# Kernel tuning notes

Measured on AMD Instinct MI355X. Metric: run time of the kernel, lower is better.

## Reference

```python
import jax, jax.numpy as jnp
import numpy as np

B, NW = 1024, 300
N = NW // 3          # 100 tokens (keypoints)
E = 5                # token dim after cat of PE(2): 3 + 2
H, D, L = 4, 64, 3   # heads, d_attention, layers


def setup_inputs() -> dict:
    key = jax.random.key(0)
    ks = jax.random.split(key, 8)
    s = jnp.float32(0.1)
    x = jax.random.normal(ks[0], (B, NW), dtype=jnp.float32)
    Wq = jax.random.normal(ks[1], (L, H, D, E), dtype=jnp.float32) * s  # per-head W_Q (no bias)
    Wk = jax.random.normal(ks[2], (L, H, D, E), dtype=jnp.float32) * s
    Wv = jax.random.normal(ks[3], (L, H, D, E), dtype=jnp.float32) * s
    Wo = jax.random.normal(ks[4], (L, E, H * D), dtype=jnp.float32) * s  # MHA output proj (no bias)
    Wf = jax.random.normal(ks[5], (L, E, E), dtype=jnp.float32) * s      # FFN linear
    bf = jax.random.normal(ks[6], (L, E), dtype=jnp.float32) * s
    g1 = jnp.ones((L, E), dtype=jnp.float32)
    b1 = jnp.zeros((L, E), dtype=jnp.float32)
    g2 = jnp.ones((L, E), dtype=jnp.float32)
    b2 = jnp.zeros((L, E), dtype=jnp.float32)
    return dict(x=x, Wq=Wq, Wk=Wk, Wv=Wv, Wo=Wo, Wf=Wf, bf=bf,
                g1=g1, b1=b1, g2=g2, b2=b2)


def _layer_norm(x, g, b, eps=1e-5):
    mu = jnp.mean(x, axis=-1, keepdims=True)
    var = jnp.mean((x - mu) ** 2, axis=-1, keepdims=True)  # biased, like torch LN
    return (x - mu) / jnp.sqrt(var + eps) * g + b


def reference(x, Wq, Wk, Wv, Wo, Wf, bf, g1, b1, g2, b2):
    kp = x.reshape(B, N, 3)                      # 'b (n d) -> b n d', d=3
    mask = kp[:, :, -1] > 0                      # [B,N] keypoint confidence mask
    # PositionalEncoding(d_model=2, kind='cat'): div_term=[1] -> pe=[sin(pos),cos(pos)]
    pos = jnp.arange(N, dtype=jnp.float32)
    pe = jnp.stack([jnp.sin(pos), jnp.cos(pos)], axis=-1)         # [N,2]
    out = jnp.concatenate([kp, jnp.broadcast_to(pe, (B, N, 2))], axis=-1)  # [B,N,5]
    out = jnp.where(mask[:, :, None], out, jnp.float32(0.0))      # out[~mask]=0

    pair = mask[:, None, None, :] & mask[:, None, :, None]        # [B,1,N,N]
    neg = -jnp.finfo(jnp.float32).max
    scale = jnp.float32(1.0 / np.sqrt(D))
    for l in range(L):
        # per-head projections (heads vectorized over h)
        q = jnp.einsum('bne,hde->bhnd', out, Wq[l])
        k = jnp.einsum('bne,hde->bhnd', out, Wk[l])
        v = jnp.einsum('bne,hde->bhnd', out, Wv[l])
        dots = jnp.einsum('bhid,bhjd->bhij', q, k) * scale        # [B,H,N,N]
        dots = jnp.where(pair, dots, neg)
        attn = jax.nn.softmax(dots, axis=-1)
        o = jnp.einsum('bhij,bhjd->bhid', attn, v)                # [B,H,N,D]
        o = o.transpose(0, 2, 1, 3).reshape(B, N, H * D)          # concat heads
        attn_out = o @ Wo[l].T                                    # [B,N,E]
        ln1 = _layer_norm(attn_out + out, g1[l], b1[l])
        ffn = jax.nn.relu(ln1 @ Wf[l].T + bf[l])
        out = _layer_norm(ffn + ln1, g2[l], b2[l])
    return out
```

## Files before the change

### kernel.cpp

```cpp
#include <hip/hip_runtime.h>
#include <math.h>

#define NTOK 100
#define EDIM 5
#define NH   4
#define NL   3
#define DD   64
#define BLK  256
#define LOG2E 1.4426950408889634f

__global__ void precompute_mp(const float* __restrict__ Wq,
                              const float* __restrict__ Wk,
                              const float* __restrict__ Wv,
                              const float* __restrict__ Wo,
                              float* __restrict__ mp) {
  const int blk = blockIdx.x;
  const int which = blk / 12;
  const int rem = blk % 12;
  const int l = rem / 4, h = rem % 4;
  const int t = threadIdx.x;

  __shared__ float A[320];
  __shared__ float Bsh[320];

  const float* wa = (which ? Wv : Wq) + (l*NH + h)*DD*EDIM;
  for (int r = t; r < 320; r += 64) A[r] = wa[r];
  if (which == 0) {
    const float* wk = Wk + (l*NH + h)*DD*EDIM;
    for (int r = t; r < 320; r += 64) Bsh[r] = wk[r];
  } else {
    for (int r = t; r < 320; r += 64) {
      int f = r >> 6, d = r & 63;
      Bsh[r] = Wo[(l*EDIM + f)*(NH*DD) + h*DD + d];
    }
  }
  __syncthreads();
  if (t < 25) {
    int e = t / 5, f = t % 5;
    float acc = 0.f;
    if (which == 0) {
      #pragma unroll 8
      for (int d = 0; d < DD; ++d) acc += A[d*5+e] * Bsh[d*5+f];
      acc *= 0.125f;
    } else {
      #pragma unroll 8
      for (int d = 0; d < DD; ++d) acc += A[d*5+e] * Bsh[f*64+d];
    }
    mp[which*960 + ((l*NH + h)*EDIM + e)*8 + f] = acc;
  }
}

__global__ __launch_bounds__(BLK, 1) void encoder_kernel(
    const float* __restrict__ x,
    const float* __restrict__ mp,
    const float* __restrict__ Wf,
    const float* __restrict__ bfv,
    const float* __restrict__ g1,
    const float* __restrict__ b1,
    const float* __restrict__ g2,
    const float* __restrict__ b2,
    float* __restrict__ out)
{
  const int wv   = threadIdx.x >> 6;
  const int lane = threadIdx.x & 63;
  const int b    = blockIdx.x * 4 + wv;

  __shared__ float s_mp[1920];
  __shared__ float s_st[4][NTOK+1][8];
  __shared__ int   s_cidx[4][NTOK];

  for (int r = threadIdx.x; r < 480; r += BLK)
    ((float4*)s_mp)[r] = ((const float4*)mp)[r];
  __syncthreads();

  float* st  = &s_st[wv][0][0];
  int* cidx  = s_cidx[wv];

  const float* xb = x + b*300;
  const int t1 = lane, t2 = lane + 64;
  float k0a = xb[3*t1], k1a = xb[3*t1+1], k2a = xb[3*t1+2];
  bool m1 = (k2a > 0.f);
  float k0b = 0.f, k1b = 0.f, k2b = 0.f; bool m2 = false;
  if (t2 < NTOK) {
    k0b = xb[3*t2]; k1b = xb[3*t2+1]; k2b = xb[3*t2+2];
    m2 = (k2b > 0.f);
  }
  unsigned long long bm1 = __ballot(m1);
  unsigned long long bm2 = __ballot(m2);
  const int pc1 = __popcll(bm1);
  const int nm  = pc1 + __popcll(bm2);
  const int ns  = nm + 1;
  unsigned long long below = (lane == 0) ? 0ull : ((1ull << lane) - 1ull);
  int p1 = __popcll(bm1 & below);
  int p2 = pc1 + __popcll(bm2 & below);
  if (m1) {
    *(float4*)(st + p1*8) = make_float4(k0a, k1a, k2a, sinf((float)t1));
    st[p1*8+4] = cosf((float)t1);
  }
  cidx[t1] = m1 ? p1 : nm;
  if (t2 < NTOK) {
    if (m2) {
      *(float4*)(st + p2*8) = make_float4(k0b, k1b, k2b, sinf((float)t2));
      st[p2*8+4] = cosf((float)t2);
    }
    cidx[t2] = m2 ? p2 : nm;
  }
  if (lane == 0) {
    *(float4*)(st + nm*8) = make_float4(0.f,0.f,0.f,0.f);
    st[nm*8+4] = 0.f;
  }

  const bool slow = (ns > 64);
  const int  rB   = lane + 64;
  const bool act1 = (lane < ns);
  const bool act2 = slow && (rB < ns);
  const bool rep1 = (lane == nm);
  const bool rep2 = (rB == nm);

  float o[5], o2[5] = {0,0,0,0,0};
  {
    float4 v = *(const float4*)(st + lane*8);
    o[0]=v.x; o[1]=v.y; o[2]=v.z; o[3]=v.w; o[4]=st[lane*8+4];
  }
  if (act2) {
    float4 v = *(const float4*)(st + rB*8);
    o2[0]=v.x; o2[1]=v.y; o2[2]=v.z; o2[3]=v.w; o2[4]=st[rB*8+4];
  }

  for (int l = 0; l < NL; ++l) {
    float a[NH][5], a2[NH][5], w[NH][5], w2[NH][5], ls[NH], ls2[NH];
    const float* Ml = s_mp + l*NH*40;

    #pragma unroll
    for (int h = 0; h < NH; ++h) {
      const float* Mh = Ml + h*40;
      float A0=0.f,A1=0.f,A2=0.f,A3=0.f,A4=0.f;
      #pragma unroll
      for (int e = 0; e < 5; ++e) {
        float4 mr = *(const float4*)(Mh + e*8);
        float  m4 = Mh[e*8+4];
        A0 += o[e]*mr.x; A1 += o[e]*mr.y; A2 += o[e]*mr.z; A3 += o[e]*mr.w; A4 += o[e]*m4;
      }
      a[h][0]=A0*LOG2E; a[h][1]=A1*LOG2E; a[h][2]=A2*LOG2E;
      a[h][3]=A3*LOG2E; a[h][4]=A4*LOG2E;
      ls[h] = 0.f;
      #pragma unroll
      for (int f = 0; f < 5; ++f) w[h][f] = 0.f;
    }
    if (slow) {
      #pragma unroll
      for (int h = 0; h < NH; ++h) {
        const float* Mh = Ml + h*40;
        float A0=0.f,A1=0.f,A2=0.f,A3=0.f,A4=0.f;
        #pragma unroll
        for (int e = 0; e < 5; ++e) {
          float4 mr = *(const float4*)(Mh + e*8);
          float  m4 = Mh[e*8+4];
          A0 += o2[e]*mr.x; A1 += o2[e]*mr.y; A2 += o2[e]*mr.z; A3 += o2[e]*mr.w; A4 += o2[e]*m4;
        }
        a2[h][0]=A0*LOG2E; a2[h][1]=A1*LOG2E; a2[h][2]=A2*LOG2E;
        a2[h][3]=A3*LOG2E; a2[h][4]=A4*LOG2E;
        ls2[h] = 0.f;
        #pragma unroll
        for (int f = 0; f < 5; ++f) w2[h][f] = 0.f;
      }
    }

    if (!slow) {
      #pragma unroll 2
      for (int j = 0; j < nm; ++j) {
        float4 oj4 = *(const float4*)(st + j*8);
        float  oj5 = st[j*8+4];
        float oj[5] = {oj4.x, oj4.y, oj4.z, oj4.w, oj5};
        #pragma unroll
        for (int h = 0; h < NH; ++h) {
          float s = a[h][0]*oj[0]+a[h][1]*oj[1]+a[h][2]*oj[2]+a[h][3]*oj[3]+a[h][4]*oj[4];
          float p = __builtin_amdgcn_exp2f(s);
          p = rep1 ? 1.f : p;
          ls[h] += p;
          #pragma unroll
          for (int e = 0; e < 5; ++e) w[h][e] += p*oj[e];
        }
      }
    } else {
      #pragma unroll 2
      for (int j = 0; j < nm; ++j) {
        float4 oj4 = *(const float4*)(st + j*8);
        float  oj5 = st[j*8+4];
        float oj[5] = {oj4.x, oj4.y, oj4.z, oj4.w, oj5};
        #pragma unroll
        for (int h = 0; h < NH; ++h) {
          float sA = a[h][0]*oj[0]+a[h][1]*oj[1]+a[h][2]*oj[2]+a[h][3]*oj[3]+a[h][4]*oj[4];
          float sB = a2[h][0]*oj[0]+a2[h][1]*oj[1]+a2[h][2]*oj[2]+a2[h][3]*oj[3]+a2[h][4]*oj[4];
          float pA = __builtin_amdgcn_exp2f(sA);
          float pB = __builtin_amdgcn_exp2f(sB);
          pB = rep2 ? 1.f : pB;
          ls[h] += pA; ls2[h] += pB;
          #pragma unroll
          for (int e = 0; e < 5; ++e) { w[h][e] += pA*oj[e]; w2[h][e] += pB*oj[e]; }
        }
      }
    }

    auto token_pass = [&](float* o_, float (*w_)[5], float* ls_,
                          bool isrep, bool active, int row) {
      float wext = isrep ? (float)(NTOK - nm) : 0.f;
      float c[5] = {0.f,0.f,0.f,0.f,0.f};
      const float* Pl = s_mp + 960 + l*NH*40;
      #pragma unroll
      for (int h = 0; h < NH; ++h) {
        float inv = isrep ? 0.01f : 1.f/ls_[h];
        const float* Ph = Pl + h*40;
        #pragma unroll
        for (int f = 0; f < 5; ++f) {
          float wn = (w_[h][f] + wext*o_[f]) * inv;
          float4 pr = *(const float4*)(Ph + f*8);
          float  p4 = Ph[f*8+4];
          c[0]+=wn*pr.x; c[1]+=wn*pr.y; c[2]+=wn*pr.z; c[3]+=wn*pr.w; c[4]+=wn*p4;
        }
      }
      float y[5];
      #pragma unroll
      for (int e = 0; e < 5; ++e) y[e] = o_[e] + c[e];
      float mu = 0.2f*(y[0]+y[1]+y[2]+y[3]+y[4]);
      float var = 0.f;
      #pragma unroll
      for (int e = 0; e < 5; ++e) { float d = y[e]-mu; var += d*d; }
      var *= 0.2f;
      float inv1 = 1.f/sqrtf(var + 1e-5f);
      float ln1[5];
      #pragma unroll
      for (int e = 0; e < 5; ++e) ln1[e] = (y[e]-mu)*inv1*g1[l*5+e] + b1[l*5+e];
      float rr[5];
      #pragma unroll
      for (int e = 0; e < 5; ++e) {
        float acc = bfv[l*5+e];
        #pragma unroll
        for (int f = 0; f < 5; ++f) acc += ln1[f]*Wf[(l*5+e)*5+f];
        acc = acc > 0.f ? acc : 0.f;
        rr[e] = acc + ln1[e];
      }
      float mu2 = 0.2f*(rr[0]+rr[1]+rr[2]+rr[3]+rr[4]);
      float var2 = 0.f;
      #pragma unroll
      for (int e = 0; e < 5; ++e) { float d = rr[e]-mu2; var2 += d*d; }
      var2 *= 0.2f;
      float inv2 = 1.f/sqrtf(var2 + 1e-5f);
      float n0 = (rr[0]-mu2)*inv2*g2[l*5+0] + b2[l*5+0];
      float n1 = (rr[1]-mu2)*inv2*g2[l*5+1] + b2[l*5+1];
      float n2 = (rr[2]-mu2)*inv2*g2[l*5+2] + b2[l*5+2];
      float n3 = (rr[3]-mu2)*inv2*g2[l*5+3] + b2[l*5+3];
      float n4 = (rr[4]-mu2)*inv2*g2[l*5+4] + b2[l*5+4];
      o_[0]=n0; o_[1]=n1; o_[2]=n2; o_[3]=n3; o_[4]=n4;
      if (active) {
        *(float4*)(st + row*8) = make_float4(n0,n1,n2,n3);
        st[row*8+4] = n4;
      }
    };
    token_pass(o,  w,  ls,  rep1, act1, lane);
    if (slow) token_pass(o2, w2, ls2, rep2, act2, rB);
  }

  const int obase = b*(NTOK*EDIM);
  #pragma unroll
  for (int rr = 0; rr < 8; ++rr) {
    int idx = rr*64 + lane;
    if (idx < NTOK*EDIM) {
      int tok = idx / 5;
      int e = idx - tok*5;
      int c = cidx[tok];
      out[obase + idx] = st[c*8 + e];
    }
  }
}

extern "C" void kernel_launch(void* const* d_in, const int* in_sizes, int n_in,
                              void* d_out, int out_size, void* d_ws, size_t ws_size,
                              hipStream_t stream) {
  const float* x  = (const float*)d_in[0];
  const float* Wq = (const float*)d_in[1];
  const float* Wk = (const float*)d_in[2];
  const float* Wv = (const float*)d_in[3];
  const float* Wo = (const float*)d_in[4];
  const float* Wf = (const float*)d_in[5];
  const float* bf = (const float*)d_in[6];
  const float* g1 = (const float*)d_in[7];
  const float* b1 = (const float*)d_in[8];
  const float* g2 = (const float*)d_in[9];
  const float* b2 = (const float*)d_in[10];
  float* outp = (float*)d_out;
  float* mp   = (float*)d_ws;

  precompute_mp<<<24, 64, 0, stream>>>(Wq, Wk, Wv, Wo, mp);
  encoder_kernel<<<256, BLK, 0, stream>>>(x, mp, Wf, bf, g1, b1, g2, b2, outp);
}
```

Baseline: 132.4 us.

## Split heads across waves with one batch element per block

Each block now processes a single batch element, with each of the four waves computing attention for one head and writing partial sums to shared memory. Wave 0 then combines heads, applies output projection, layer norms and FFN, and block-wide barriers separate the phases. The grid grows from 256 to 1024 blocks to expose more waves and shorter per-wave attention loops. It adds per-layer synchronisation and leaves three waves idle during the token pass.

```diff
diff --git a/kernel.cpp b/kernel.cpp
--- a/kernel.cpp
+++ b/kernel.cpp
@@ -50,7 +50,7 @@
   }
 }
 
-__global__ __launch_bounds__(BLK, 1) void encoder_kernel(
+__global__ __launch_bounds__(BLK) void encoder_kernel(
     const float* __restrict__ x,
     const float* __restrict__ mp,
     const float* __restrict__ Wf,
@@ -63,18 +63,15 @@
 {
   const int wv   = threadIdx.x >> 6;
   const int lane = threadIdx.x & 63;
-  const int b    = blockIdx.x * 4 + wv;
+  const int b    = blockIdx.x;
 
   __shared__ float s_mp[1920];
-  __shared__ float s_st[4][NTOK+1][8];
-  __shared__ int   s_cidx[4][NTOK];
+  __shared__ float s_st[104][8];
+  __shared__ float s_w[NH][104][8];
+  __shared__ int   s_cidx[NTOK];
 
   for (int r = threadIdx.x; r < 480; r += BLK)
     ((float4*)s_mp)[r] = ((const float4*)mp)[r];
-  __syncthreads();
-
-  float* st  = &s_st[wv][0][0];
-  int* cidx  = s_cidx[wv];
 
   const float* xb = x + b*300;
   const int t1 = lane, t2 = lane + 64;
@@ -90,187 +87,144 @@
   const int pc1 = __popcll(bm1);
   const int nm  = pc1 + __popcll(bm2);
   const int ns  = nm + 1;
-  unsigned long long below = (lane == 0) ? 0ull : ((1ull << lane) - 1ull);
-  int p1 = __popcll(bm1 & below);
-  int p2 = pc1 + __popcll(bm2 & below);
-  if (m1) {
-    *(float4*)(st + p1*8) = make_float4(k0a, k1a, k2a, sinf((float)t1));
-    st[p1*8+4] = cosf((float)t1);
-  }
-  cidx[t1] = m1 ? p1 : nm;
-  if (t2 < NTOK) {
-    if (m2) {
-      *(float4*)(st + p2*8) = make_float4(k0b, k1b, k2b, sinf((float)t2));
-      st[p2*8+4] = cosf((float)t2);
-    }
-    cidx[t2] = m2 ? p2 : nm;
-  }
-  if (lane == 0) {
-    *(float4*)(st + nm*8) = make_float4(0.f,0.f,0.f,0.f);
-    st[nm*8+4] = 0.f;
-  }
-
-  const bool slow = (ns > 64);
-  const int  rB   = lane + 64;
-  const bool act1 = (lane < ns);
-  const bool act2 = slow && (rB < ns);
-  const bool rep1 = (lane == nm);
-  const bool rep2 = (rB == nm);
-
-  float o[5], o2[5] = {0,0,0,0,0};
-  {
-    float4 v = *(const float4*)(st + lane*8);
-    o[0]=v.x; o[1]=v.y; o[2]=v.z; o[3]=v.w; o[4]=st[lane*8+4];
-  }
-  if (act2) {
-    float4 v = *(const float4*)(st + rB*8);
-    o2[0]=v.x; o2[1]=v.y; o2[2]=v.z; o2[3]=v.w; o2[4]=st[rB*8+4];
-  }
+  if (wv == 0) {
+    unsigned long long below = (lane == 0) ? 0ull : ((1ull << lane) - 1ull);
+    int p1 = __popcll(bm1 & below);
+    int p2 = pc1 + __popcll(bm2 & below);
+    if (m1) {
+      *(float4*)(&s_st[p1][0]) = make_float4(k0a, k1a, k2a, sinf((float)t1));
+      s_st[p1][4] = cosf((float)t1);
+    }
+    s_cidx[t1] = m1 ? p1 : nm;
+    if (t2 < NTOK) {
+      if (m2) {
+        *(float4*)(&s_st[p2][0]) = make_float4(k0b, k1b, k2b, sinf((float)t2));
+        s_st[p2][4] = cosf((float)t2);
+      }
+      s_cidx[t2] = m2 ? p2 : nm;
+    }
+    if (lane == 0) {
+      *(float4*)(&s_st[nm][0]) = make_float4(0.f,0.f,0.f,0.f);
+      s_st[nm][4] = 0.f;
+    }
+  }
+  __syncthreads();
+
+  const int nh2 = (ns > 64) ? 2 : 1;
 
   for (int l = 0; l < NL; ++l) {
-    float a[NH][5], a2[NH][5], w[NH][5], w2[NH][5], ls[NH], ls2[NH];
-    const float* Ml = s_mp + l*NH*40;
-
-    #pragma unroll
-    for (int h = 0; h < NH; ++h) {
-      const float* Mh = Ml + h*40;
-      float A0=0.f,A1=0.f,A2=0.f,A3=0.f,A4=0.f;
+    for (int half = 0; half < nh2; ++half) {
+      const int row = lane + (half << 6);
+      const bool active = (row < ns);
+      const bool rep = (row == nm);
+      const int rr = active ? row : 0;
+
+      float4 ov = *(const float4*)(&s_st[rr][0]);
+      float o[5] = {ov.x, ov.y, ov.z, ov.w, s_st[rr][4]};
+
+      const float* Mh = s_mp + (l*NH + wv)*40;
+      float a0=0.f,a1=0.f,a2=0.f,a3=0.f,a4=0.f;
       #pragma unroll
       for (int e = 0; e < 5; ++e) {
         float4 mr = *(const float4*)(Mh + e*8);
         float  m4 = Mh[e*8+4];
-        A0 += o[e]*mr.x; A1 += o[e]*mr.y; A2 += o[e]*mr.z; A3 += o[e]*mr.w; A4 += o[e]*m4;
-      }
-      a[h][0]=A0*LOG2E; a[h][1]=A1*LOG2E; a[h][2]=A2*LOG2E;
-      a[h][3]=A3*LOG2E; a[h][4]=A4*LOG2E;
-      ls[h] = 0.f;
-      #pragma unroll
-      for (int f = 0; f < 5; ++f) w[h][f] = 0.f;
-    }
-    if (slow) {
-      #pragma unroll
-      for (int h = 0; h < NH; ++h) {
-        const float* Mh = Ml + h*40;
-        float A0=0.f,A1=0.f,A2=0.f,A3=0.f,A4=0.f;
+        a0 += o[e]*mr.x; a1 += o[e]*mr.y; a2 += o[e]*mr.z; a3 += o[e]*mr.w; a4 += o[e]*m4;
+      }
+      a0*=LOG2E; a1*=LOG2E; a2*=LOG2E; a3*=LOG2E; a4*=LOG2E;
+
+      float ls=0.f, w0=0.f,w1=0.f,w2=0.f,w3=0.f,w4=0.f;
+      #pragma unroll 4
+      for (int j = 0; j < nm; ++j) {
+        float4 oj = *(const float4*)(&s_st[j][0]);
+        float  oe = s_st[j][4];
+        float s = a0*oj.x + a1*oj.y + a2*oj.z + a3*oj.w + a4*oe;
+        float p = __builtin_amdgcn_exp2f(s);
+        p = rep ? 1.f : p;
+        ls += p;
+        w0 += p*oj.x; w1 += p*oj.y; w2 += p*oj.z; w3 += p*oj.w; w4 += p*oe;
+      }
+      if (active) {
+        *(float4*)(&s_w[wv][row][0]) = make_float4(w0, w1, w2, w3);
+        *(float2*)(&s_w[wv][row][4]) = make_float2(w4, ls);
+      }
+    }
+    __syncthreads();
+
+    if (wv == 0) {
+      for (int half = 0; half < nh2; ++half) {
+        const int row = lane + (half << 6);
+        const bool active = (row < ns);
+        const bool rep = (row == nm);
+        const int rr = active ? row : 0;
+
+        float4 ov = *(const float4*)(&s_st[rr][0]);
+        float o[5] = {ov.x, ov.y, ov.z, ov.w, s_st[rr][4]};
+        float wext = rep ? (float)(NTOK - nm) : 0.f;
+
+        float c[5] = {0.f,0.f,0.f,0.f,0.f};
+        const float* Pl = s_mp + 960 + l*NH*40;
+        #pragma unroll
+        for (int h = 0; h < NH; ++h) {
+          float4 wa = *(const float4*)(&s_w[h][rr][0]);
+          float2 wb = *(const float2*)(&s_w[h][rr][4]);
+          float w[5] = {wa.x, wa.y, wa.z, wa.w, wb.x};
+          float inv = rep ? 0.01f : 1.f/wb.y;
+          const float* Ph = Pl + h*40;
+          #pragma unroll
+          for (int f = 0; f < 5; ++f) {
+            float wn = (w[f] + wext*o[f]) * inv;
+            float4 pr = *(const float4*)(Ph + f*8);
+            float  p4 = Ph[f*8+4];
+            c[0]+=wn*pr.x; c[1]+=wn*pr.y; c[2]+=wn*pr.z; c[3]+=wn*pr.w; c[4]+=wn*p4;
+          }
+        }
+        float y[5];
+        #pragma unroll
+        for (int e = 0; e < 5; ++e) y[e] = o[e] + c[e];
+        float mu = 0.2f*(y[0]+y[1]+y[2]+y[3]+y[4]);
+        float var = 0.f;
+        #pragma unroll
+        for (int e = 0; e < 5; ++e) { float d = y[e]-mu; var += d*d; }
+        var *= 0.2f;
+        float inv1 = 1.f/sqrtf(var + 1e-5f);
+        float ln1[5];
+        #pragma unroll
+        for (int e = 0; e < 5; ++e) ln1[e] = (y[e]-mu)*inv1*g1[l*5+e] + b1[l*5+e];
+        float rv[5];
         #pragma unroll
         for (int e = 0; e < 5; ++e) {
-          float4 mr = *(const float4*)(Mh + e*8);
-          float  m4 = Mh[e*8+4];
-          A0 += o2[e]*mr.x; A1 += o2[e]*mr.y; A2 += o2[e]*mr.z; A3 += o2[e]*mr.w; A4 += o2[e]*m4;
+          float acc = bfv[l*5+e];
+          #pragma unroll
+          for (int f = 0; f < 5; ++f) acc += ln1[f]*Wf[(l*5+e)*5+f];
+          acc = acc > 0.f ? acc : 0.f;
+          rv[e] = acc + ln1[e];
         }
-        a2[h][0]=A0*LOG2E; a2[h][1]=A1*LOG2E; a2[h][2]=A2*LOG2E;
-        a2[h][3]=A3*LOG2E; a2[h][4]=A4*LOG2E;
-        ls2[h] = 0.f;
-        #pragma unroll
-        for (int f = 0; f < 5; ++f) w2[h][f] = 0.f;
-      }
-    }
-
-    if (!slow) {
-      #pragma unroll 2
-      for (int j = 0; j < nm; ++j) {
-        float4 oj4 = *(const float4*)(st + j*8);
-        float  oj5 = st[j*8+4];
-        float oj[5] = {oj4.x, oj4.y, oj4.z, oj4.w, oj5};
-        #pragma unroll
-        for (int h = 0; h < NH; ++h) {
-          float s = a[h][0]*oj[0]+a[h][1]*oj[1]+a[h][2]*oj[2]+a[h][3]*oj[3]+a[h][4]*oj[4];
-          float p = __builtin_amdgcn_exp2f(s);
-          p = rep1 ? 1.f : p;
-          ls[h] += p;
-          #pragma unroll
-          for (int e = 0; e < 5; ++e) w[h][e] += p*oj[e];
+        float mu2 = 0.2f*(rv[0]+rv[1]+rv[2]+rv[3]+rv[4]);
+        float var2 = 0.f;
+        #pragma unroll
+        for (int e = 0; e < 5; ++e) { float d = rv[e]-mu2; var2 += d*d; }
+        var2 *= 0.2f;
+        float inv2 = 1.f/sqrtf(var2 + 1e-5f);
+        float n0 = (rv[0]-mu2)*inv2*g2[l*5+0] + b2[l*5+0];
+        float n1 = (rv[1]-mu2)*inv2*g2[l*5+1] + b2[l*5+1];
+        float n2 = (rv[2]-mu2)*inv2*g2[l*5+2] + b2[l*5+2];
+        float n3 = (rv[3]-mu2)*inv2*g2[l*5+3] + b2[l*5+3];
+        float n4 = (rv[4]-mu2)*inv2*g2[l*5+4] + b2[l*5+4];
+        if (active) {
+          *(float4*)(&s_st[row][0]) = make_float4(n0, n1, n2, n3);
+          s_st[row][4] = n4;
         }
       }
-    } else {
-      #pragma unroll 2
-      for (int j = 0; j < nm; ++j) {
-        float4 oj4 = *(const float4*)(st + j*8);
-        float  oj5 = st[j*8+4];
-        float oj[5] = {oj4.x, oj4.y, oj4.z, oj4.w, oj5};
-        #pragma unroll
-        for (int h = 0; h < NH; ++h) {
-          float sA = a[h][0]*oj[0]+a[h][1]*oj[1]+a[h][2]*oj[2]+a[h][3]*oj[3]+a[h][4]*oj[4];
-          float sB = a2[h][0]*oj[0]+a2[h][1]*oj[1]+a2[h][2]*oj[2]+a2[h][3]*oj[3]+a2[h][4]*oj[4];
-          float pA = __builtin_amdgcn_exp2f(sA);
-          float pB = __builtin_amdgcn_exp2f(sB);
-          pB = rep2 ? 1.f : pB;
-          ls[h] += pA; ls2[h] += pB;
-          #pragma unroll
-          for (int e = 0; e < 5; ++e) { w[h][e] += pA*oj[e]; w2[h][e] += pB*oj[e]; }
-        }
-      }
-    }
-
-    auto token_pass = [&](float* o_, float (*w_)[5], float* ls_,
-                          bool isrep, bool active, int row) {
-      float wext = isrep ? (float)(NTOK - nm) : 0.f;
-      float c[5] = {0.f,0.f,0.f,0.f,0.f};
-      const float* Pl = s_mp + 960 + l*NH*40;
-      #pragma unroll
-      for (int h = 0; h < NH; ++h) {
-        float inv = isrep ? 0.01f : 1.f/ls_[h];
-        const float* Ph = Pl + h*40;
-        #pragma unroll
-        for (int f = 0; f < 5; ++f) {
-          float wn = (w_[h][f] + wext*o_[f]) * inv;
-          float4 pr = *(const float4*)(Ph + f*8);
-          float  p4 = Ph[f*8+4];
-          c[0]+=wn*pr.x; c[1]+=wn*pr.y; c[2]+=wn*pr.z; c[3]+=wn*pr.w; c[4]+=wn*p4;
-        }
-      }
-      float y[5];
-      #pragma unroll
-      for (int e = 0; e < 5; ++e) y[e] = o_[e] + c[e];
-      float mu = 0.2f*(y[0]+y[1]+y[2]+y[3]+y[4]);
-      float var = 0.f;
-      #pragma unroll
-      for (int e = 0; e < 5; ++e) { float d = y[e]-mu; var += d*d; }
-      var *= 0.2f;
-      float inv1 = 1.f/sqrtf(var + 1e-5f);
-      float ln1[5];
-      #pragma unroll
-      for (int e = 0; e < 5; ++e) ln1[e] = (y[e]-mu)*inv1*g1[l*5+e] + b1[l*5+e];
-      float rr[5];
-      #pragma unroll
-      for (int e = 0; e < 5; ++e) {
-        float acc = bfv[l*5+e];
-        #pragma unroll
-        for (int f = 0; f < 5; ++f) acc += ln1[f]*Wf[(l*5+e)*5+f];
-        acc = acc > 0.f ? acc : 0.f;
-        rr[e] = acc + ln1[e];
-      }
-      float mu2 = 0.2f*(rr[0]+rr[1]+rr[2]+rr[3]+rr[4]);
-      float var2 = 0.f;
-      #pragma unroll
-      for (int e = 0; e < 5; ++e) { float d = rr[e]-mu2; var2 += d*d; }
-      var2 *= 0.2f;
-      float inv2 = 1.f/sqrtf(var2 + 1e-5f);
-      float n0 = (rr[0]-mu2)*inv2*g2[l*5+0] + b2[l*5+0];
-      float n1 = (rr[1]-mu2)*inv2*g2[l*5+1] + b2[l*5+1];
-      float n2 = (rr[2]-mu2)*inv2*g2[l*5+2] + b2[l*5+2];
-      float n3 = (rr[3]-mu2)*inv2*g2[l*5+3] + b2[l*5+3];
-      float n4 = (rr[4]-mu2)*inv2*g2[l*5+4] + b2[l*5+4];
-      o_[0]=n0; o_[1]=n1; o_[2]=n2; o_[3]=n3; o_[4]=n4;
-      if (active) {
-        *(float4*)(st + row*8) = make_float4(n0,n1,n2,n3);
-        st[row*8+4] = n4;
-      }
-    };
-    token_pass(o,  w,  ls,  rep1, act1, lane);
-    if (slow) token_pass(o2, w2, ls2, rep2, act2, rB);
+    }
+    __syncthreads();
   }
 
   const int obase = b*(NTOK*EDIM);
-  #pragma unroll
-  for (int rr = 0; rr < 8; ++rr) {
-    int idx = rr*64 + lane;
-    if (idx < NTOK*EDIM) {
-      int tok = idx / 5;
-      int e = idx - tok*5;
-      int c = cidx[tok];
-      out[obase + idx] = st[c*8 + e];
-    }
+  for (int idx = threadIdx.x; idx < NTOK*EDIM; idx += BLK) {
+    int tok = idx / 5;
+    int e = idx - tok*5;
+    int c = s_cidx[tok];
+    out[obase + idx] = s_st[c][e];
   }
 }
 
@@ -292,5 +246,5 @@
   float* mp   = (float*)d_ws;
 
   precompute_mp<<<24, 64, 0, stream>>>(Wq, Wk, Wv, Wo, mp);
-  encoder_kernel<<<256, BLK, 0, stream>>>(x, mp, Wf, bf, g1, b1, g2, b2, outp);
+  encoder_kernel<<<1024, BLK, 0, stream>>>(x, mp, Wf, bf, g1, b1, g2, b2, outp);
 }
```

Measured after the change: 128.2 us. 1.03x faster.
